# Performance work log

Measured on AMD Instinct MI355X. Metric: run time of the kernel, lower is better.

## Reference

```python
import jax, jax.numpy as jnp
import numpy as np

T, K, H, E, I = 128, 8, 2048, 64, 768


def setup_inputs() -> dict:
    key = jax.random.key(0)
    k1, k2, k3, k4, k5, k6 = jax.random.split(key, 6)
    return {
        "hidden_states": jax.random.normal(k1, (T, H), dtype=jnp.float32),
        "top_k_index": jax.random.randint(k2, (T, K), 0, E, dtype=jnp.int64),
        "top_k_weights": jax.random.uniform(k3, (T, K), dtype=jnp.float32),
        "w_gate": jax.random.normal(k4, (E, H, I), dtype=jnp.float32) * 0.02,
        "w_up": jax.random.normal(k5, (E, H, I), dtype=jnp.float32) * 0.02,
        "w_down": jax.random.normal(k6, (E, I, H), dtype=jnp.float32) * 0.02,
    }


def reference(hidden_states, top_k_index, top_k_weights, w_gate, w_up, w_down):
    # Per-token routed SwiGLU experts (Qwen3.5 MoE expert block):
    #   out_t = sum_k w_tk * down_{e_tk}( silu(gate_{e_tk}(x_t)) * up_{e_tk}(x_t) )
    h = hidden_states.astype(jnp.float32)  # [T, H]
    gate = jnp.einsum("td,edh->eth", h, w_gate)  # [E, T, I]
    up = jnp.einsum("td,edh->eth", h, w_up)      # [E, T, I]
    act = jax.nn.silu(gate) * up                 # [E, T, I]
    out_all = jnp.einsum("eti,eih->eth", act, w_down)  # [E, T, H]
    t_idx = jnp.arange(h.shape[0])
    sel = out_all[top_k_index, t_idx[:, None]]   # [T, K, H]
    out = jnp.sum(sel * top_k_weights[..., None], axis=1)  # [T, H]
    return out
```

## Files before the change

### kernel.cpp

```cpp
#include <hip/hip_runtime.h>
#include <stdint.h>

constexpr int Tn = 128;
constexpr int Kn = 8;
constexpr int Hn = 2048;
constexpr int En = 64;
constexpr int In = 768;
constexpr int NP = Tn * Kn;
constexpr int NTI = In / 128;

__global__ void route_kernel(const int* __restrict__ idx32,
                             int* __restrict__ offsets,
                             int* __restrict__ entries) {
  __shared__ int s_cnt[En];
  __shared__ int s_cur[En];
  __shared__ int s_odd_or;
  const int tid = threadIdx.x;
  if (tid == 0) s_odd_or = 0;
  if (tid < En) s_cnt[tid] = 0;
  __syncthreads();
  if (tid < NP / 2) {
    if (idx32[2 * tid + 1] != 0) atomicOr(&s_odd_or, 1);
  }
  __syncthreads();
  const bool is64 = (s_odd_or == 0);
  const int e = is64 ? idx32[2 * tid] : idx32[tid];
  atomicAdd(&s_cnt[e], 1);
  __syncthreads();
  if (tid == 0) {
    int acc = 0;
    for (int i = 0; i < En; ++i) { s_cur[i] = acc; offsets[i] = acc; acc += s_cnt[i]; }
    offsets[En] = acc;
  }
  __syncthreads();
  const int pos = atomicAdd(&s_cur[e], 1);
  entries[pos] = tid;
}

__global__ __launch_bounds__(256, 2) void gateup_mono(
    const float* __restrict__ hs, const float* __restrict__ wg,
    const float* __restrict__ wu, const int* __restrict__ offsets,
    const int* __restrict__ entries, float* __restrict__ gu) {
  const int b = blockIdx.x;
  const int tile = b % NTI;
  const int em = b / NTI;
  const int e = em & 63;
  const int m = em >> 6;
  const int beg = offsets[e];
  const int cnt = offsets[e + 1] - beg;
  if (cnt == 0) return;

  const int wave = threadIdx.x >> 6;
  const int lane = threadIdx.x & 63;
  const int col = tile * 128 + lane * 2;

  __shared__ float s_h[32][64];
  __shared__ int s_tok[32];

  const float* W = m ? wu : wg;
  const float* wp = W + (size_t)e * Hn * In + col;
  float* gup = gu + (size_t)m * NP * In;

  for (int chunk = 0; chunk < cnt; chunk += 32) {
    __syncthreads();
    if (threadIdx.x < 32) {
      const int r = threadIdx.x;
      s_tok[r] = entries[beg + chunk + min(r, cnt - chunk - 1)] >> 3;
    }
    __syncthreads();

    float2 acc[8];
#pragma unroll
    for (int j = 0; j < 8; ++j) acc[j] = make_float2(0.f, 0.f);

    for (int d0 = 0; d0 < Hn; d0 += 64) {
      {
        const int r = threadIdx.x >> 3;
        const int g = (threadIdx.x & 7) * 8;
        const float* src = hs + (size_t)s_tok[r] * Hn + d0 + g;
        const float4 a = *reinterpret_cast<const float4*>(src);
        const float4 b4 = *reinterpret_cast<const float4*>(src + 4);
        *reinterpret_cast<float4*>(&s_h[r][g]) = a;
        *reinterpret_cast<float4*>(&s_h[r][g + 4]) = b4;
      }
      __syncthreads();
      const float* wdd = wp + (size_t)d0 * In;
#pragma unroll 2
      for (int dg = 0; dg < 64; dg += 4) {
        float2 wv[4];
#pragma unroll
        for (int q = 0; q < 4; ++q)
          wv[q] = *reinterpret_cast<const float2*>(wdd + (size_t)(dg + q) * In);
#pragma unroll
        for (int j = 0; j < 8; ++j) {
          const float4 hv = *reinterpret_cast<const float4*>(&s_h[wave * 8 + j][dg]);
          const float hvv[4] = {hv.x, hv.y, hv.z, hv.w};
#pragma unroll
          for (int q = 0; q < 4; ++q) {
            acc[j].x = fmaf(hvv[q], wv[q].x, acc[j].x);
            acc[j].y = fmaf(hvv[q], wv[q].y, acc[j].y);
          }
        }
      }
      __syncthreads();
    }

#pragma unroll
    for (int j = 0; j < 8; ++j) {
      const int r = wave * 8 + j;
      if (chunk + r < cnt) {
        *reinterpret_cast<float2*>(&gup[(size_t)(beg + chunk + r) * In + col]) =
            acc[j];
      }
    }
  }
}

__global__ void silu_kernel(float* __restrict__ gu) {
  const int i = blockIdx.x * blockDim.x + threadIdx.x;
  float4* g4 = reinterpret_cast<float4*>(gu);
  const float4* u4 = reinterpret_cast<const float4*>(gu + (size_t)NP * In);
  float4 g = g4[i];
  const float4 u = u4[i];
  g.x = g.x / (1.f + __expf(-g.x)) * u.x;
  g.y = g.y / (1.f + __expf(-g.y)) * u.y;
  g.z = g.z / (1.f + __expf(-g.z)) * u.z;
  g.w = g.w / (1.f + __expf(-g.w)) * u.w;
  g4[i] = g;
}

__global__ __launch_bounds__(256, 2) void down_kernel(
    const float* __restrict__ act, const float* __restrict__ wd,
    const float* __restrict__ tkw, const int* __restrict__ offsets,
    const int* __restrict__ entries, float* __restrict__ out) {
  const int e = blockIdx.x >> 4;
  const int tile = blockIdx.x & 15;
  const int beg = offsets[e];
  const int cnt = offsets[e + 1] - beg;
  if (cnt == 0) return;

  const int wave = threadIdx.x >> 6;
  const int lane = threadIdx.x & 63;
  const int col = tile * 128 + lane * 2;

  __shared__ float s_a[32][64];
  __shared__ int s_tok[32];
  __shared__ int s_arow[32];
  __shared__ float s_w[32];

  const float* wdp = wd + (size_t)e * In * Hn + col;

  for (int chunk = 0; chunk < cnt; chunk += 32) {
    __syncthreads();
    if (threadIdx.x < 32) {
      const int r = threadIdx.x;
      const int rr = min(r, cnt - chunk - 1);
      const int p = entries[beg + chunk + rr];
      s_tok[r] = p >> 3;
      s_w[r] = tkw[p];
      s_arow[r] = beg + chunk + rr;
    }
    __syncthreads();

    float2 acc[8];
#pragma unroll
    for (int j = 0; j < 8; ++j) acc[j] = make_float2(0.f, 0.f);

    for (int i0 = 0; i0 < In; i0 += 64) {
      {
        const int r = threadIdx.x >> 3;
        const int g = (threadIdx.x & 7) * 8;
        const float* src = act + (size_t)s_arow[r] * In + i0 + g;
        const float4 a = *reinterpret_cast<const float4*>(src);
        const float4 b4 = *reinterpret_cast<const float4*>(src + 4);
        *reinterpret_cast<float4*>(&s_a[r][g]) = a;
        *reinterpret_cast<float4*>(&s_a[r][g + 4]) = b4;
      }
      __syncthreads();
      const float* wdi = wdp + (size_t)i0 * Hn;
#pragma unroll 2
      for (int ig = 0; ig < 64; ig += 4) {
        float2 wdv[4];
#pragma unroll
        for (int q = 0; q < 4; ++q)
          wdv[q] = *reinterpret_cast<const float2*>(wdi + (size_t)(ig + q) * Hn);
#pragma unroll
        for (int j = 0; j < 8; ++j) {
          const float4 av = *reinterpret_cast<const float4*>(&s_a[wave * 8 + j][ig]);
          const float avv[4] = {av.x, av.y, av.z, av.w};
#pragma unroll
          for (int q = 0; q < 4; ++q) {
            acc[j].x = fmaf(avv[q], wdv[q].x, acc[j].x);
            acc[j].y = fmaf(avv[q], wdv[q].y, acc[j].y);
          }
        }
      }
      __syncthreads();
    }

#pragma unroll
    for (int j = 0; j < 8; ++j) {
      const int r = wave * 8 + j;
      if (chunk + r < cnt) {
        const float w = s_w[r];
        float* op = out + (size_t)s_tok[r] * Hn + col;
        atomicAdd(op, w * acc[j].x);
        atomicAdd(op + 1, w * acc[j].y);
      }
    }
  }
}

extern "C" void kernel_launch(void* const* d_in, const int* in_sizes, int n_in,
                              void* d_out, int out_size, void* d_ws, size_t ws_size,
                              hipStream_t stream) {
  const float* hs  = (const float*)d_in[0];
  const int*   idx = (const int*)d_in[1];
  const float* tkw = (const float*)d_in[2];
  const float* wg  = (const float*)d_in[3];
  const float* wu  = (const float*)d_in[4];
  const float* wd  = (const float*)d_in[5];
  float* out = (float*)d_out;

  char* ws = (char*)d_ws;
  int* offsets = (int*)ws;
  int* entries = (int*)(ws + 512);
  float* gu    = (float*)(ws + 8192);

  route_kernel<<<1, NP, 0, stream>>>(idx, offsets, entries);
  hipMemsetAsync(d_out, 0, (size_t)Tn * Hn * sizeof(float), stream);
  gateup_mono<<<2 * En * NTI, 256, 0, stream>>>(hs, wg, wu, offsets, entries, gu);
  silu_kernel<<<NP * In / 4 / 256, 256, 0, stream>>>(gu);
  down_kernel<<<En * (Hn / 128), 256, 0, stream>>>(gu, wd, tkw, offsets, entries, out);
}
```

Baseline: 452.9 us.

## Split gate/up GEMM over hidden dimension with single-wave blocks and atomic accumulation

Rewrites the gate/up projection kernel so each 64-thread block handles a 256-column tile, one eighth of the hidden dimension, and one of four row groups. Hidden-state rows are read directly from global memory with wave-uniform token pointers instead of being staged through shared memory, which removes the block barriers. Partial sums are combined with float atomics into a zeroed buffer, which needs an extra memset. The goal is far more blocks in flight to keep the weight stream saturated, at the cost of atomic traffic and re-reading activations once per column tile.

```diff
diff --git a/kernel.cpp b/kernel.cpp
--- a/kernel.cpp
+++ b/kernel.cpp
@@ -7,7 +7,10 @@
 constexpr int En = 64;
 constexpr int In = 768;
 constexpr int NP = Tn * Kn;
-constexpr int NTI = In / 128;
+constexpr int CT = 3;
+constexpr int GDS = 8;
+constexpr int GDSL = Hn / GDS;
+constexpr int NRG = 4;
 
 __global__ void route_kernel(const int* __restrict__ idx32,
                              int* __restrict__ offsets,
@@ -37,80 +40,76 @@
   entries[pos] = tid;
 }
 
-__global__ __launch_bounds__(256, 2) void gateup_mono(
+__global__ __launch_bounds__(64, 8) void gateup_scalar(
     const float* __restrict__ hs, const float* __restrict__ wg,
     const float* __restrict__ wu, const int* __restrict__ offsets,
     const int* __restrict__ entries, float* __restrict__ gu) {
   const int b = blockIdx.x;
-  const int tile = b % NTI;
-  const int em = b / NTI;
+  const int rg0 = b & (NRG - 1);
+  const int ds = (b >> 2) & (GDS - 1);
+  const int tile = (b >> 5) % CT;
+  const int em = (b >> 5) / CT;
   const int e = em & 63;
   const int m = em >> 6;
   const int beg = offsets[e];
   const int cnt = offsets[e + 1] - beg;
-  if (cnt == 0) return;
-
-  const int wave = threadIdx.x >> 6;
-  const int lane = threadIdx.x & 63;
-  const int col = tile * 128 + lane * 2;
-
-  __shared__ float s_h[32][64];
-  __shared__ int s_tok[32];
+  if (cnt == 0 || rg0 * 8 >= cnt) return;
+
+  const int lane = threadIdx.x;
+  const int col = tile * 256 + lane * 4;
+  const int dbeg = ds * GDSL;
 
   const float* W = m ? wu : wg;
-  const float* wp = W + (size_t)e * Hn * In + col;
+  const float* wp = W + ((size_t)e * Hn + dbeg) * In + col;
   float* gup = gu + (size_t)m * NP * In;
 
-  for (int chunk = 0; chunk < cnt; chunk += 32) {
-    __syncthreads();
-    if (threadIdx.x < 32) {
-      const int r = threadIdx.x;
-      s_tok[r] = entries[beg + chunk + min(r, cnt - chunk - 1)] >> 3;
-    }
-    __syncthreads();
-
-    float2 acc[8];
-#pragma unroll
-    for (int j = 0; j < 8; ++j) acc[j] = make_float2(0.f, 0.f);
-
-    for (int d0 = 0; d0 < Hn; d0 += 64) {
-      {
-        const int r = threadIdx.x >> 3;
-        const int g = (threadIdx.x & 7) * 8;
-        const float* src = hs + (size_t)s_tok[r] * Hn + d0 + g;
-        const float4 a = *reinterpret_cast<const float4*>(src);
-        const float4 b4 = *reinterpret_cast<const float4*>(src + 4);
-        *reinterpret_cast<float4*>(&s_h[r][g]) = a;
-        *reinterpret_cast<float4*>(&s_h[r][g + 4]) = b4;
-      }
-      __syncthreads();
-      const float* wdd = wp + (size_t)d0 * In;
-#pragma unroll 2
-      for (int dg = 0; dg < 64; dg += 4) {
-        float2 wv[4];
-#pragma unroll
-        for (int q = 0; q < 4; ++q)
-          wv[q] = *reinterpret_cast<const float2*>(wdd + (size_t)(dg + q) * In);
+  for (int r0 = rg0 * 8; r0 < cnt; r0 += NRG * 8) {
+    const float* hr[8];
+#pragma unroll
+    for (int j = 0; j < 8; ++j) {
+      const int p = entries[beg + r0 + min(j, cnt - 1 - r0)];
+      const int tk = __builtin_amdgcn_readfirstlane(p >> 3);
+      hr[j] = hs + (size_t)tk * Hn + dbeg;
+    }
+
+    float4 acc[8];
+#pragma unroll
+    for (int j = 0; j < 8; ++j) acc[j] = make_float4(0.f, 0.f, 0.f, 0.f);
+
+    for (int dg = 0; dg < GDSL; dg += 8) {
+      float4 wv[8];
+#pragma unroll
+      for (int q = 0; q < 8; ++q)
+        wv[q] = *reinterpret_cast<const float4*>(wp + (size_t)(dg + q) * In);
+      float4 h0[8], h1[8];
+#pragma unroll
+      for (int j = 0; j < 8; ++j) {
+        h0[j] = *reinterpret_cast<const float4*>(hr[j] + dg);
+        h1[j] = *reinterpret_cast<const float4*>(hr[j] + dg + 4);
+      }
+#pragma unroll
+      for (int q = 0; q < 8; ++q) {
 #pragma unroll
         for (int j = 0; j < 8; ++j) {
-          const float4 hv = *reinterpret_cast<const float4*>(&s_h[wave * 8 + j][dg]);
-          const float hvv[4] = {hv.x, hv.y, hv.z, hv.w};
-#pragma unroll
-          for (int q = 0; q < 4; ++q) {
-            acc[j].x = fmaf(hvv[q], wv[q].x, acc[j].x);
-            acc[j].y = fmaf(hvv[q], wv[q].y, acc[j].y);
-          }
+          const float4 hv4 = (q < 4) ? h0[j] : h1[j];
+          const float h =
+              (q & 3) == 0 ? hv4.x : (q & 3) == 1 ? hv4.y : (q & 3) == 2 ? hv4.z : hv4.w;
+          acc[j].x = fmaf(h, wv[q].x, acc[j].x);
+          acc[j].y = fmaf(h, wv[q].y, acc[j].y);
+          acc[j].z = fmaf(h, wv[q].z, acc[j].z);
+          acc[j].w = fmaf(h, wv[q].w, acc[j].w);
         }
       }
-      __syncthreads();
     }
 
 #pragma unroll
     for (int j = 0; j < 8; ++j) {
-      const int r = wave * 8 + j;
-      if (chunk + r < cnt) {
-        *reinterpret_cast<float2*>(&gup[(size_t)(beg + chunk + r) * In + col]) =
-            acc[j];
+      if (r0 + j < cnt) {
+        const size_t ap = (size_t)(beg + r0 + j) * In + col;
+        atomicAdd(&gup[ap], acc[j].x);
+        atomicAdd(&gup[ap + 1], acc[j].y);
+        atomicAdd(&gup[ap + 2], acc[j].z);
+        atomicAdd(&gup[ap + 3], acc[j].w);
       }
     }
   }
@@ -226,10 +225,13 @@
   int* offsets = (int*)ws;
   int* entries = (int*)(ws + 512);
   float* gu    = (float*)(ws + 8192);
+  const size_t gu_bytes = (size_t)2 * NP * In * sizeof(float);
 
   route_kernel<<<1, NP, 0, stream>>>(idx, offsets, entries);
   hipMemsetAsync(d_out, 0, (size_t)Tn * Hn * sizeof(float), stream);
-  gateup_mono<<<2 * En * NTI, 256, 0, stream>>>(hs, wg, wu, offsets, entries, gu);
+  hipMemsetAsync(gu, 0, gu_bytes, stream);
+  gateup_scalar<<<2 * En * CT * GDS * NRG, 64, 0, stream>>>(hs, wg, wu, offsets,
+                                                            entries, gu);
   silu_kernel<<<NP * In / 4 / 256, 256, 0, stream>>>(gu);
   down_kernel<<<En * (Hn / 128), 256, 0, stream>>>(gu, wd, tkw, offsets, entries, out);
 }
```

After: 599.9 us. 1.32x slower.
